# Optimization experiments

Measured on AMD Instinct MI355X. Metric: run time of the kernel, lower is better.

Reference implementation:

```python
import jax, jax.numpy as jnp
import numpy as np
from jax import lax

B, CIN, COUT, H, W = 4, 256, 256, 64, 64
KH = KW = 3
STRIDE = PAD = DIL = 1
GROUPS = 1
K = KH * KW
HO = (H + 2 * PAD - DIL * (KH - 1) - 1) // STRIDE + 1
WO = (W + 2 * PAD - DIL * (KW - 1) - 1) // STRIDE + 1
DN = ('NCHW', 'OIHW', 'NCHW')


def _sep_conv(x, dw, pw):
    # Separable2d: depthwise kxk conv (stride/pad/dilation) then pointwise 1x1.
    y = lax.conv_general_dilated(x, dw, (STRIDE, STRIDE), [(PAD, PAD), (PAD, PAD)],
                                 rhs_dilation=(DIL, DIL), feature_group_count=x.shape[1],
                                 dimension_numbers=DN)
    return lax.conv_general_dilated(y, pw, (1, 1), 'VALID', dimension_numbers=DN)


def _deform_conv2d(x, offset, mask, weight, bias):
    Bb, Cin, Hh, Ww = x.shape
    O = weight.shape[0]
    G = offset.shape[1] // (2 * K)  # offset groups
    offs = offset.reshape(Bb, G, K, 2, HO, WO)
    dy, dx = offs[:, :, :, 0], offs[:, :, :, 1]  # [B,G,K,Ho,Wo]
    ki, kj = jnp.meshgrid(jnp.arange(KH), jnp.arange(KW), indexing='ij')
    base_y = (-PAD + ki.reshape(K, 1) * DIL + jnp.arange(HO)[None, :] * STRIDE).astype(x.dtype)  # [K,Ho]
    base_x = (-PAD + kj.reshape(K, 1) * DIL + jnp.arange(WO)[None, :] * STRIDE).astype(x.dtype)  # [K,Wo]
    py = base_y[None, None, :, :, None] + dy  # [B,G,K,Ho,Wo]
    px = base_x[None, None, :, None, :] + dx

    xg = x.reshape(Bb, G, Cin // G, Hh, Ww)

    def bilinear(img, py, px):
        # img [C,H,W], py/px [K,Ho,Wo]; zero-padding outside bounds.
        y0 = jnp.floor(py)
        x0 = jnp.floor(px)
        out = jnp.zeros((img.shape[0],) + py.shape, img.dtype)
        for a, (iy, wy) in enumerate((((y0), (y0 + 1 - py)), ((y0 + 1), (py - y0)))):
            for b, (ix, wx) in enumerate((((x0), (x0 + 1 - px)), ((x0 + 1), (px - x0)))):
                valid = (iy >= 0) & (iy < Hh) & (ix >= 0) & (ix < Ww)
                iyc = jnp.clip(iy, 0, Hh - 1).astype(jnp.int32)
                ixc = jnp.clip(ix, 0, Ww - 1).astype(jnp.int32)
                v = img[:, iyc, ixc]  # [C,K,Ho,Wo]
                out = out + v * (wy * wx * valid)[None]
        return out

    sampled = jax.vmap(jax.vmap(bilinear))(xg, py, px)  # [B,G,C/G,K,Ho,Wo]
    m = mask.reshape(Bb, G, K, HO, WO)
    sampled = sampled * m[:, :, None]

    cols = sampled.reshape(Bb, Cin, K, HO, WO).reshape(Bb, GROUPS, Cin // GROUPS, K, HO, WO)
    wr = weight.reshape(GROUPS, O // GROUPS, Cin // GROUPS, K)
    out = jnp.einsum('bgckhw,gock->bgohw', cols, wr).reshape(Bb, O, HO, WO)
    return out + bias[None, :, None, None]


def setup_inputs() -> dict:
    key = jax.random.key(0)
    ks = jax.random.split(key, 7)
    x = jax.random.normal(ks[0], (B, CIN, H, W), jnp.float32)
    weight = jax.random.normal(ks[1], (COUT, CIN // GROUPS, KH, KW), jnp.float32) / np.sqrt(CIN * K)
    bias = jax.random.normal(ks[2], (COUT,), jnp.float32) * 0.01
    off_dw = jax.random.normal(ks[3], (CIN, 1, KH, KW), jnp.float32) * 0.01
    off_pw = jax.random.normal(ks[4], (2 * K * GROUPS, CIN, 1, 1), jnp.float32) * 0.01
    mask_dw = jax.random.normal(ks[5], (CIN, 1, KH, KW), jnp.float32) * 0.01
    mask_pw = jax.random.normal(ks[6], (K * GROUPS, CIN, 1, 1), jnp.float32) * 0.01
    return dict(x=x, weight=weight, bias=bias, off_dw=off_dw, off_pw=off_pw,
                mask_dw=mask_dw, mask_pw=mask_pw)


def reference(x, weight, bias, off_dw, off_pw, mask_dw, mask_pw):
    offset = _sep_conv(x, off_dw, off_pw)                       # [B,2*K,Ho,Wo]
    mask = jax.nn.sigmoid(_sep_conv(x, mask_dw, mask_pw)) * 2.0  # MaskSigmoid(scale=2)
    return _deform_conv2d(x, offset, mask, weight, bias)
```

## Files before the change

### kernel.cpp

```cpp
#include <hip/hip_runtime.h>

#define CIN   256
#define COUT  256
#define HH    64
#define WW    64
#define KD    2304
#define NPIX  16384
#define SPLIT 8
#define CPS   (CIN / SPLIT)
#define NSTEP 18

typedef __attribute__((ext_vector_type(4))) float  float4v;
typedef __attribute__((ext_vector_type(4))) unsigned int uint4v;
typedef _Float16 h2 __attribute__((ext_vector_type(2)));
typedef _Float16 h8 __attribute__((ext_vector_type(8)));
typedef unsigned int u32;
typedef unsigned short u16;

__device__ __forceinline__ h2 as_h2(u32 v) { union { u32 u; h2 h; } x; x.u = v; return x.h; }
__device__ __forceinline__ u32 as_u32(h2 h) { union { u32 u; h2 h; } x; x.h = h; return x.u; }
__device__ __forceinline__ u16 f2h_bits(float f) { _Float16 h = (_Float16)f; return *(u16*)&h; }

__device__ __forceinline__ void gload_lds16(const void* g, void* l) {
  __builtin_amdgcn_global_load_lds((const __attribute__((address_space(1))) u32*)g,
                                   (__attribute__((address_space(3))) u32*)l, 16, 0, 0);
}

__global__ __launch_bounds__(256) void offmask_part_kernel(
    const float* __restrict__ x,
    const float* __restrict__ off_dw, const float* __restrict__ off_pw,
    const float* __restrict__ mask_dw, const float* __restrict__ mask_pw,
    float* __restrict__ part)
{
  int m = blockIdx.x * 256 + threadIdx.x;
  int s = blockIdx.y;
  int b = m >> 12, pix = m & 4095;
  int ho = pix >> 6, wo = pix & 63;
  const float* xb = x + (size_t)b * CIN * 4096;

  float acc[27];
#pragma unroll
  for (int j = 0; j < 27; ++j) acc[j] = 0.f;

  int c0 = s * CPS;
  for (int ci = 0; ci < CPS; ++ci) {
    int c = c0 + ci;
    const float* xc = xb + (size_t)c * 4096;
    float d_off = 0.f, d_msk = 0.f;
#pragma unroll
    for (int t = 0; t < 9; ++t) {
      int gy = ho + t / 3 - 1, gx = wo + t % 3 - 1;
      bool ok = (gy >= 0) & (gy < HH) & (gx >= 0) & (gx < WW);
      float v = ok ? xc[gy * 64 + gx] : 0.f;
      d_off += v * off_dw[c * 9 + t];
      d_msk += v * mask_dw[c * 9 + t];
    }
#pragma unroll
    for (int j = 0; j < 18; ++j) acc[j] += d_off * off_pw[j * 256 + c];
#pragma unroll
    for (int j = 0; j < 9; ++j) acc[18 + j] += d_msk * mask_pw[j * 256 + c];
  }
  float* pp = part + ((size_t)s * NPIX + m) * 32;
#pragma unroll
  for (int j = 0; j < 27; ++j) pp[j] = acc[j];
}

__global__ __launch_bounds__(256) void offmask_reduce_kernel(
    const float* __restrict__ part, float* __restrict__ rec)
{
  int i = blockIdx.x * 256 + threadIdx.x;
  int m = i >> 5, j = i & 31;
  if (j >= 27) { rec[i] = 0.f; return; }
  float sum = 0.f;
#pragma unroll
  for (int s = 0; s < SPLIT; ++s) sum += part[((size_t)s * NPIX + m) * 32 + j];
  rec[i] = (j < 18) ? sum : 2.f / (1.f + __expf(-sum));
}

__global__ __launch_bounds__(256) void wconv_kernel(const float* __restrict__ w,
                                                    u16* __restrict__ wb)
{
  int i = blockIdx.x * 256 + threadIdx.x;
  int co = i / KD, rem = i - co * KD;
  int c = rem / 9, kk = rem - c * 9;
  wb[co * KD + kk * 256 + c] = f2h_bits(w[i]);
}

__global__ __launch_bounds__(256) void xpose_kernel(const float* __restrict__ x,
                                                    u16* __restrict__ xt)
{
  __shared__ float t[64][65];
  int ptile = blockIdx.x;
  int ctile = blockIdx.y;
  int b     = blockIdx.z;
  int tid = threadIdx.x;
  const float* xb = x + (size_t)b * CIN * 4096 + (size_t)ctile * 64 * 4096 + ptile * 64;
#pragma unroll
  for (int i = 0; i < 16; ++i) {
    int c = i * 4 + (tid >> 6), p = tid & 63;
    t[c][p] = xb[(size_t)c * 4096 + p];
  }
  __syncthreads();
  u16* xo = xt + ((size_t)b * 4096 + ptile * 64) * 256 + ctile * 64;
#pragma unroll
  for (int i = 0; i < 16; ++i) {
    int p = i * 4 + (tid >> 6), c = tid & 63;
    xo[(size_t)p * 256 + c] = f2h_bits(t[c][p]);
  }
}

__global__ __launch_bounds__(512, 2) void gemm_fused_kernel(
    const u16* __restrict__ A,
    const u16* __restrict__ xt,
    const float* __restrict__ rec,
    const float* __restrict__ bias,
    float* __restrict__ out,
    float* __restrict__ tmp)
{
  __shared__ __align__(16) u16 lA[3][256 * 32];
  __shared__ __align__(16) u16 lB[2][256 * 32];
  const int tid = threadIdx.x;
  const int ord = blockIdx.x;
  const int xcd = ord & 7, slot = ord >> 3;
  const int ptile = (slot >> 2) * 8 + xcd;
  const int h     = slot & 3;
  const int m0  = ptile * 256;
  const int b_img = ptile >> 4;
  const int cbase = h * 64;
  const int wave = tid >> 6, lane = tid & 63;
  const int wm = wave >> 1, wn = wave & 1;
  const int rl = lane & 15, kq = lane >> 4;
  const int sA = (kq ^ (rl & 3) ^ ((rl >> 2) & 3)) * 8;

  const int rA  = tid >> 2;
  const int koA = ((tid & 3) ^ (rA & 3) ^ ((rA >> 2) & 3)) * 8;
  const u16* aRow0 = A + (size_t)rA * KD + koA;
  const u16* aRow1 = A + (size_t)(rA + 128) * KD + koA;

  const int px_t = tid >> 1;
  const int chh  = (tid & 1) * 16;
  const int m_px = m0 + px_t;
  const int ho = (m_px & 4095) >> 6, wo = m_px & 63;
  const float* rp = rec + (size_t)m_px * 32;
  const u16* xb = xt + (size_t)b_img * 4096 * 256;
  const int swzp = (px_t & 3) ^ ((px_t >> 2) & 3);
  const int wAddr0 = px_t * 32 + ((((tid & 1) * 2)     ^ swzp) * 8);
  const int wAddr1 = px_t * 32 + ((((tid & 1) * 2 + 1) ^ swzp) * 8);

  u32 cOff[4];
  h2  wh[4];

#define KCOL(t_) (((t_) >> 1) * 256 + cbase + ((t_) & 1) * 32)

#define CALC_CORNERS(kk_) do {                                             \
    float dy = rp[(kk_) * 2], dx = rp[(kk_) * 2 + 1], msk = rp[18 + (kk_)];\
    float py  = (float)(ho - 1 + ((kk_) / 3)) + dy;                        \
    float pxf = (float)(wo - 1 + ((kk_) % 3)) + dx;                        \
    float fy = floorf(py), fx = floorf(pxf);                               \
    int y0 = (int)fy, x0 = (int)fx;                                        \
    float wy1 = py - fy, wy0 = 1.f - wy1;                                  \
    float wx1 = pxf - fx, wx0 = 1.f - wx1;                                 \
    _Pragma("unroll")                                                      \
    for (int cr = 0; cr < 4; ++cr) {                                       \
      int iy = y0 + (cr >> 1), ix = x0 + (cr & 1);                         \
      bool valid = (iy >= 0) & (iy < HH) & (ix >= 0) & (ix < WW);          \
      int iyc = min(max(iy, 0), HH - 1), ixc = min(max(ix, 0), WW - 1);    \
      cOff[cr] = (u32)(iyc * 64 + ixc) * 256;                              \
      float wy = (cr >> 1) ? wy1 : wy0;                                    \
      float wx = (cr & 1) ? wx1 : wx0;                                     \
      float wf = valid ? (wy * wx * msk) : 0.f;                            \
      _Float16 hw = (_Float16)wf;                                          \
      wh[cr] = (h2){hw, hw};                                               \
    }                                                                      \
  } while (0)

#define STAGE_A(k_, slot_) do {                                            \
    int k0_ = KCOL(k_);                                                    \
    gload_lds16(aRow0 + k0_, lA[slot_] + tid * 8);                         \
    gload_lds16(aRow1 + k0_, lA[slot_] + (tid + 512) * 8);                 \
  } while (0)

#define SAMP_LOAD(t_, va, vb) do {                                         \
    int c0n_ = cbase + ((t_) & 1) * 32 + chh;                              \
    _Pragma("unroll")                                                      \
    for (int cr = 0; cr < 4; ++cr) {                                       \
      va[cr] = *(const uint4v*)(xb + cOff[cr] + c0n_);                     \
      vb[cr] = *(const uint4v*)(xb + cOff[cr] + c0n_ + 8);                 \
    }                                                                      \
  } while (0)

#define BLEND_WRITE(bufi_, va, vb) do {                                    \
    uint4v o0, o1;                                                         \
    _Pragma("unroll")                                                      \
    for (int w_ = 0; w_ < 4; ++w_) {                                       \
      h2 s0_ = wh[0] * as_h2(va[0][w_]) + wh[1] * as_h2(va[1][w_]);        \
      s0_   += wh[2] * as_h2(va[2][w_]) + wh[3] * as_h2(va[3][w_]);        \
      h2 s1_ = wh[0] * as_h2(vb[0][w_]) + wh[1] * as_h2(vb[1][w_]);        \
      s1_   += wh[2] * as_h2(vb[2][w_]) + wh[3] * as_h2(vb[3][w_]);        \
      o0[w_] = as_u32(s0_); o1[w_] = as_u32(s1_);                          \
    }                                                                      \
    *(uint4v*)&lB[bufi_][wAddr0] = o0;                                     \
    *(uint4v*)&lB[bufi_][wAddr1] = o1;                                     \
  } while (0)

  float4v acc[4][8];
#pragma unroll
  for (int m = 0; m < 4; ++m)
#pragma unroll
    for (int n = 0; n < 8; ++n) acc[m][n] = float4v{0.f, 0.f, 0.f, 0.f};

  {
    CALC_CORNERS(0);
    uint4v va[4], vb[4];
    SAMP_LOAD(0, va, vb);
    STAGE_A(0, 0);
    STAGE_A(1, 1);
    asm volatile("s_waitcnt vmcnt(2)" ::: "memory");
    BLEND_WRITE(0, va, vb);
    asm volatile("s_waitcnt lgkmcnt(0)" ::: "memory");
    __builtin_amdgcn_s_barrier();
  }

  for (int it = 0; it < 3; ++it) {
#pragma unroll
    for (int u = 0; u < 6; ++u) {
      const int t = it * 6 + u;
      const int tn  = (t + 1 == NSTEP) ? 0 : t + 1;
      const int tn2 = (t + 2 >= NSTEP) ? (t + 2 - NSTEP) : t + 2;
      if ((tn & 1) == 0) CALC_CORNERS(tn >> 1);
      uint4v va[4], vb[4];
      SAMP_LOAD(tn, va, vb);
      STAGE_A(tn2, (u + 2) % 3);
      h8 af[4], bf[8];
#pragma unroll
      for (int m = 0; m < 4; ++m)
        af[m] = *(const h8*)&lA[u % 3][(wm * 64 + m * 16 + rl) * 32 + sA];
#pragma unroll
      for (int n = 0; n < 8; ++n)
        bf[n] = *(const h8*)&lB[u & 1][(wn * 128 + n * 16 + rl) * 32 + sA];
#pragma unroll
      for (int m = 0; m < 4; ++m)
#pragma unroll
        for (int n = 0; n < 8; ++n)
          acc[m][n] = __builtin_amdgcn_mfma_f32_16x16x32_f16(af[m], bf[n], acc[m][n], 0, 0, 0);
      asm volatile("s_waitcnt vmcnt(2)" ::: "memory");
      BLEND_WRITE((u + 1) & 1, va, vb);
      asm volatile("s_waitcnt lgkmcnt(0)" ::: "memory");
      __builtin_amdgcn_s_barrier();
    }
  }
#undef STAGE_A
#undef CALC_CORNERS
#undef SAMP_LOAD
#undef BLEND_WRITE
#undef KCOL

  const int p_base = (m0 & 4095) + wn * 128;
  float* db = (h ? (tmp + (size_t)(h - 1) * COUT * NPIX) : out) +
              (size_t)b_img * COUT * 4096;
#pragma unroll
  for (int m = 0; m < 4; ++m) {
#pragma unroll
    for (int j = 0; j < 4; ++j) {
      int co = wm * 64 + m * 16 + kq * 4 + j;
      float bv = h ? 0.f : bias[co];
#pragma unroll
      for (int n = 0; n < 8; ++n) {
        int pp = p_base + n * 16 + rl;
        db[(size_t)co * 4096 + pp] = acc[m][n][j] + bv;
      }
    }
  }
}

__global__ __launch_bounds__(256) void add_kernel(float* __restrict__ out,
                                                  const float* __restrict__ tmp)
{
  size_t i = ((size_t)blockIdx.x * 256 + threadIdx.x) * 4;
  float4v a  = *(const float4v*)(out + i);
  float4v b0 = *(const float4v*)(tmp + i);
  float4v b1 = *(const float4v*)(tmp + (size_t)COUT * NPIX + i);
  float4v b2 = *(const float4v*)(tmp + (size_t)2 * COUT * NPIX + i);
  a += b0 + b1 + b2;
  *(float4v*)(out + i) = a;
}

extern "C" void kernel_launch(void* const* d_in, const int* in_sizes, int n_in,
                              void* d_out, int out_size, void* d_ws, size_t ws_size,
                              hipStream_t stream) {
  const float* x       = (const float*)d_in[0];
  const float* weight  = (const float*)d_in[1];
  const float* bias    = (const float*)d_in[2];
  const float* off_dw  = (const float*)d_in[3];
  const float* off_pw  = (const float*)d_in[4];
  const float* mask_dw = (const float*)d_in[5];
  const float* mask_pw = (const float*)d_in[6];

  if (ws_size < 61997056ull) return;
  float* rec  = (float*)d_ws;
  u16*   wb   = (u16*)((char*)d_ws + 2097152);
  u16*   xt   = (u16*)((char*)d_ws + 3276800);
  float* part = (float*)((char*)d_ws + 11665408);
  float* tmp  = part;
  float* out  = (float*)d_out;

  wconv_kernel<<<dim3(2304), dim3(256), 0, stream>>>(weight, wb);
  offmask_part_kernel<<<dim3(NPIX / 256, SPLIT), dim3(256), 0, stream>>>(
      x, off_dw, off_pw, mask_dw, mask_pw, part);
  offmask_reduce_kernel<<<dim3(NPIX * 32 / 256), dim3(256), 0, stream>>>(part, rec);
  xpose_kernel<<<dim3(64, 4, 4), dim3(256), 0, stream>>>(x, xt);
  gemm_fused_kernel<<<dim3(256), dim3(512), 0, stream>>>(wb, xt, rec, bias, out, tmp);
  add_kernel<<<dim3(COUT * NPIX / 4 / 256), dim3(256), 0, stream>>>(out, tmp);
}
```

Baseline: 109.6 us.

## Store split-K partials in fp16 and double offset/mask channel split

The offset/mask partial sums are now packed as fp16 pairs in 16-word rows, and the channel split goes from 8 to 16 so more blocks run in parallel. All four split-K GEMM slices now write fp16 partials to a workspace instead of fp32. Bias addition moves into the final reduction kernel, which sums four fp16 slices and writes fp32 output. The aim is to cut global memory traffic for the partial buffers, at the cost of fp16 rounding in intermediate sums, which may loosen accuracy.

```diff
diff --git a/kernel.cpp b/kernel.cpp
--- a/kernel.cpp
+++ b/kernel.cpp
@@ -6,7 +6,7 @@
 #define WW    64
 #define KD    2304
 #define NPIX  16384
-#define SPLIT 8
+#define SPLIT 16
 #define CPS   (CIN / SPLIT)
 #define NSTEP 18
 
@@ -20,6 +20,10 @@
 __device__ __forceinline__ h2 as_h2(u32 v) { union { u32 u; h2 h; } x; x.u = v; return x.h; }
 __device__ __forceinline__ u32 as_u32(h2 h) { union { u32 u; h2 h; } x; x.h = h; return x.u; }
 __device__ __forceinline__ u16 f2h_bits(float f) { _Float16 h = (_Float16)f; return *(u16*)&h; }
+__device__ __forceinline__ float h2f(u16 b) { _Float16 h = *(_Float16*)&b; return (float)h; }
+__device__ __forceinline__ u32 packh2(float a, float b) {
+  h2 h; h[0] = (_Float16)a; h[1] = (_Float16)b; return as_u32(h);
+}
 
 __device__ __forceinline__ void gload_lds16(const void* g, void* l) {
   __builtin_amdgcn_global_load_lds((const __attribute__((address_space(1))) u32*)g,
@@ -30,7 +34,7 @@
     const float* __restrict__ x,
     const float* __restrict__ off_dw, const float* __restrict__ off_pw,
     const float* __restrict__ mask_dw, const float* __restrict__ mask_pw,
-    float* __restrict__ part)
+    u32* __restrict__ part2)
 {
   int m = blockIdx.x * 256 + threadIdx.x;
   int s = blockIdx.y;
@@ -60,21 +64,31 @@
 #pragma unroll
     for (int j = 0; j < 9; ++j) acc[18 + j] += d_msk * mask_pw[j * 256 + c];
   }
-  float* pp = part + ((size_t)s * NPIX + m) * 32;
-#pragma unroll
-  for (int j = 0; j < 27; ++j) pp[j] = acc[j];
+  uint4v o[4];
+#pragma unroll
+  for (int k = 0; k < 13; ++k) o[k >> 2][k & 3] = packh2(acc[2 * k], acc[2 * k + 1]);
+  o[3][1] = packh2(acc[26], 0.f);
+  o[3][2] = 0; o[3][3] = 0;
+  uint4v* pp = (uint4v*)(part2 + ((size_t)s * NPIX + m) * 16);
+#pragma unroll
+  for (int q = 0; q < 4; ++q) pp[q] = o[q];
 }
 
 __global__ __launch_bounds__(256) void offmask_reduce_kernel(
-    const float* __restrict__ part, float* __restrict__ rec)
+    const u32* __restrict__ part2, float* __restrict__ rec)
 {
   int i = blockIdx.x * 256 + threadIdx.x;
-  int m = i >> 5, j = i & 31;
-  if (j >= 27) { rec[i] = 0.f; return; }
-  float sum = 0.f;
-#pragma unroll
-  for (int s = 0; s < SPLIT; ++s) sum += part[((size_t)s * NPIX + m) * 32 + j];
-  rec[i] = (j < 18) ? sum : 2.f / (1.f + __expf(-sum));
+  int m = i >> 4, k = i & 15;
+  int j0 = 2 * k, j1 = 2 * k + 1;
+  if (j0 >= 27) { rec[(size_t)m * 32 + j0] = 0.f; rec[(size_t)m * 32 + j1] = 0.f; return; }
+  float s0 = 0.f, s1 = 0.f;
+#pragma unroll
+  for (int s = 0; s < SPLIT; ++s) {
+    h2 v = as_h2(part2[((size_t)s * NPIX + m) * 16 + k]);
+    s0 += (float)v[0]; s1 += (float)v[1];
+  }
+  rec[(size_t)m * 32 + j0] = (j0 < 18) ? s0 : 2.f / (1.f + __expf(-s0));
+  rec[(size_t)m * 32 + j1] = (j1 < 18) ? s1 : ((j1 < 27) ? 2.f / (1.f + __expf(-s1)) : 0.f);
 }
 
 __global__ __launch_bounds__(256) void wconv_kernel(const float* __restrict__ w,
@@ -113,9 +127,7 @@
     const u16* __restrict__ A,
     const u16* __restrict__ xt,
     const float* __restrict__ rec,
-    const float* __restrict__ bias,
-    float* __restrict__ out,
-    float* __restrict__ tmp)
+    u16* __restrict__ tmp4)
 {
   __shared__ __align__(16) u16 lA[3][256 * 32];
   __shared__ __align__(16) u16 lB[2][256 * 32];
@@ -256,33 +268,43 @@
 #undef KCOL
 
   const int p_base = (m0 & 4095) + wn * 128;
-  float* db = (h ? (tmp + (size_t)(h - 1) * COUT * NPIX) : out) +
-              (size_t)b_img * COUT * 4096;
+  u16* db = tmp4 + (size_t)h * COUT * NPIX + (size_t)b_img * COUT * 4096;
 #pragma unroll
   for (int m = 0; m < 4; ++m) {
 #pragma unroll
     for (int j = 0; j < 4; ++j) {
       int co = wm * 64 + m * 16 + kq * 4 + j;
-      float bv = h ? 0.f : bias[co];
 #pragma unroll
       for (int n = 0; n < 8; ++n) {
         int pp = p_base + n * 16 + rl;
-        db[(size_t)co * 4096 + pp] = acc[m][n][j] + bv;
+        db[(size_t)co * 4096 + pp] = f2h_bits(acc[m][n][j]);
       }
     }
   }
 }
 
-__global__ __launch_bounds__(256) void add_kernel(float* __restrict__ out,
-                                                  const float* __restrict__ tmp)
-{
-  size_t i = ((size_t)blockIdx.x * 256 + threadIdx.x) * 4;
-  float4v a  = *(const float4v*)(out + i);
-  float4v b0 = *(const float4v*)(tmp + i);
-  float4v b1 = *(const float4v*)(tmp + (size_t)COUT * NPIX + i);
-  float4v b2 = *(const float4v*)(tmp + (size_t)2 * COUT * NPIX + i);
-  a += b0 + b1 + b2;
-  *(float4v*)(out + i) = a;
+__global__ __launch_bounds__(256) void add_kernel(const u16* __restrict__ tmp4,
+                                                  const float* __restrict__ bias,
+                                                  float* __restrict__ out)
+{
+  size_t i = ((size_t)blockIdx.x * 256 + threadIdx.x) * 8;
+  int co = (int)((i >> 12) & 255);
+  float bv = bias[co];
+  uint4v v0 = *(const uint4v*)(tmp4 + i);
+  uint4v v1 = *(const uint4v*)(tmp4 + (size_t)COUT * NPIX + i);
+  uint4v v2 = *(const uint4v*)(tmp4 + (size_t)2 * COUT * NPIX + i);
+  uint4v v3 = *(const uint4v*)(tmp4 + (size_t)3 * COUT * NPIX + i);
+  float4v oA, oB;
+#pragma unroll
+  for (int w = 0; w < 4; ++w) {
+    h2 a = as_h2(v0[w]), b = as_h2(v1[w]), c = as_h2(v2[w]), d = as_h2(v3[w]);
+    float lo = (float)a[0] + (float)b[0] + (float)c[0] + (float)d[0] + bv;
+    float hi = (float)a[1] + (float)b[1] + (float)c[1] + (float)d[1] + bv;
+    if (w < 2) { oA[w * 2] = lo; oA[w * 2 + 1] = hi; }
+    else       { oB[(w - 2) * 2] = lo; oB[(w - 2) * 2 + 1] = hi; }
+  }
+  *(float4v*)(out + i) = oA;
+  *(float4v*)(out + i + 4) = oB;
 }
 
 extern "C" void kernel_launch(void* const* d_in, const int* in_sizes, int n_in,
@@ -296,19 +318,19 @@
   const float* mask_dw = (const float*)d_in[5];
   const float* mask_pw = (const float*)d_in[6];
 
-  if (ws_size < 61997056ull) return;
-  float* rec  = (float*)d_ws;
-  u16*   wb   = (u16*)((char*)d_ws + 2097152);
-  u16*   xt   = (u16*)((char*)d_ws + 3276800);
-  float* part = (float*)((char*)d_ws + 11665408);
-  float* tmp  = part;
-  float* out  = (float*)d_out;
+  if (ws_size < 45219840ull) return;
+  float* rec   = (float*)d_ws;
+  u16*   wb    = (u16*)((char*)d_ws + 2097152);
+  u16*   xt    = (u16*)((char*)d_ws + 3276800);
+  u32*   part2 = (u32*)((char*)d_ws + 11665408);
+  u16*   tmp4  = (u16*)((char*)d_ws + 11665408);
+  float* out   = (float*)d_out;
 
   wconv_kernel<<<dim3(2304), dim3(256), 0, stream>>>(weight, wb);
   offmask_part_kernel<<<dim3(NPIX / 256, SPLIT), dim3(256), 0, stream>>>(
-      x, off_dw, off_pw, mask_dw, mask_pw, part);
-  offmask_reduce_kernel<<<dim3(NPIX * 32 / 256), dim3(256), 0, stream>>>(part, rec);
+      x, off_dw, off_pw, mask_dw, mask_pw, part2);
+  offmask_reduce_kernel<<<dim3(NPIX * 16 / 256), dim3(256), 0, stream>>>(part2, rec);
   xpose_kernel<<<dim3(64, 4, 4), dim3(256), 0, stream>>>(x, xt);
-  gemm_fused_kernel<<<dim3(256), dim3(512), 0, stream>>>(wb, xt, rec, bias, out, tmp);
-  add_kernel<<<dim3(COUT * NPIX / 4 / 256), dim3(256), 0, stream>>>(out, tmp);
-}
+  gemm_fused_kernel<<<dim3(256), dim3(512), 0, stream>>>(wb, xt, rec, tmp4);
+  add_kernel<<<dim3(COUT * NPIX / 8 / 256), dim3(256), 0, stream>>>(tmp4, bias, out);
+}
```

New measurement: 92.89 us. 15.2% less time.
